# Optimization experiments

Hardware: AMD Instinct MI355X
Metric: run time of the kernel (lower is better)

Reference implementation:

```python
import jax, jax.numpy as jnp
import numpy as np

TS = (32, 32, 32)          # tensor_size per dim
NC = 32 * 32 * 32          # total grid cells
HEADS = 4


def setup_inputs() -> dict:
    key = jax.random.key(0)
    k1, k2, k3 = jax.random.split(key, 3)
    B, H, V, N = 4, HEADS, 8, 16384
    local_coordinate = jax.random.uniform(k1, (B, H, V, N), dtype=jnp.float32)
    flattened_index = jax.random.randint(k2, (B, H, V, N), 0, NC, dtype=jnp.int64)
    features = jax.random.normal(k3, (B, 128, N), dtype=jnp.float32)
    return {"local_coordinate": local_coordinate,
            "flattened_index": flattened_index,
            "features": features}


def reference(local_coordinate, flattened_index, features):
    # local_coordinate: [B, H, V, N], flattened_index: [B, H, V, N] int64
    # features: [B, H*fd, N]
    B, H, V, N = local_coordinate.shape
    fd = features.shape[1] // H
    feats = features.reshape(B, H, fd, N)
    # outer-product splat: [B, H, fd, V, N]
    pre_splat = feats[:, :, :, None, :] * local_coordinate[:, :, None, :, :]
    src = pre_splat.reshape(B, H, fd, V * N)
    idx = flattened_index.reshape(B, H, V * N)

    def scat(s, i):
        # s: [fd, V*N], i: [V*N]; out initialized to zeros like torch scatter_max with zero out
        return jnp.zeros((fd, NC), dtype=s.dtype).at[:, i].max(s)

    z = jax.vmap(jax.vmap(scat))(src, idx)  # [B, H, fd, NC]
    return z.reshape(B, H * fd, *TS)
```

## Files before the change

kernel.cpp:

```cpp
#include <hip/hip_runtime.h>
#include <hip/hip_bf16.h>

constexpr int B  = 4;
constexpr int H  = 4;
constexpr int V  = 8;
constexpr int N  = 16384;
constexpr int FD = 32;
constexpr int NC = 32768;
constexpr int BH = B * H;
constexpr int VN = V * N;
constexpr int NPAIR = BH * VN;

constexpr int CB   = 1024;
constexpr int CAPB = 208;
constexpr int TP   = 8192;
constexpr int SB   = NPAIR / TP;
constexpr int TB   = BH * (N / 128);

constexpr size_t OFF_BCNT   = 0;
constexpr size_t OFF_SLOTS  = OFF_BCNT  + (size_t)BH * CB;
constexpr size_t OFF_FEATST = OFF_SLOTS + (size_t)BH * CB * CAPB;

__device__ __forceinline__ unsigned short f2bf(float v) {
    unsigned int u = __float_as_uint(v);
    return (unsigned short)((u + 0x7FFFu + ((u >> 16) & 1u)) >> 16);
}

__global__ __launch_bounds__(1024)
void k_prep(const int* __restrict__ idx, const float* __restrict__ lc,
            const float* __restrict__ feats, int* __restrict__ bcnt,
            unsigned int* __restrict__ slots, unsigned short* __restrict__ featsT) {
    __shared__ __align__(16) unsigned char smem[61440];
    const int tid = threadIdx.x;

    if (blockIdx.x < SB) {
        unsigned int*   skey   = (unsigned int*)smem;
        unsigned short* scb    = (unsigned short*)(smem + 32768);
        int*            s      = (int*)(smem + 49152);
        int*            cursor = (int*)(smem + 53248);
        int*            rbase  = (int*)(smem + 57344);

        const size_t t0 = (size_t)blockIdx.x * TP;
        const int bh = (int)(t0 >> 17);

        s[tid] = 0;
        __syncthreads();

        const int4* idx4 = (const int4*)(idx + t0);
        int4 c4a[2];
#pragma unroll
        for (int r = 0; r < 2; ++r) {
            int4 c4 = idx4[tid + r * 1024];
            c4a[r] = c4;
            atomicAdd(&s[c4.x >> 5], 1);
            atomicAdd(&s[c4.y >> 5], 1);
            atomicAdd(&s[c4.z >> 5], 1);
            atomicAdd(&s[c4.w >> 5], 1);
        }
        __syncthreads();
        const int myc = s[tid];

        for (int off = 1; off < 1024; off <<= 1) {
            int v = (tid >= off) ? s[tid - off] : 0;
            __syncthreads();
            s[tid] += v;
            __syncthreads();
        }
        const int scanstart = s[tid] - myc;
        __syncthreads();
        s[tid]      = scanstart;
        cursor[tid] = scanstart;
        rbase[tid]  = (myc > 0) ? atomicAdd(&bcnt[bh * CB + tid], myc) : 0;
        __syncthreads();

        const float4* lc4 = (const float4*)(lc + t0);
        const unsigned int nb = (unsigned int)(t0 & (N - 1));
#pragma unroll
        for (int r = 0; r < 2; ++r) {
            int i = tid + r * 1024;
            int4   c4 = c4a[r];
            float4 l4 = lc4[i];
            unsigned int n0 = nb + (unsigned int)(i * 4);
            int cx[4] = {c4.x, c4.y, c4.z, c4.w};
            float lx[4] = {l4.x, l4.y, l4.z, l4.w};
#pragma unroll
            for (int e = 0; e < 4; ++e) {
                unsigned int q = (unsigned int)(lx[e] * 8192.0f);
                unsigned int key = ((unsigned int)(cx[e] & 31) << 27)
                                 | (q << 14) | (n0 + e);
                int cb = cx[e] >> 5;
                int pos = atomicAdd(&cursor[cb], 1);
                skey[pos] = key;
                scb[pos]  = (unsigned short)cb;
            }
        }
        __syncthreads();

#pragma unroll
        for (int r = 0; r < 8; ++r) {
            int j  = tid + r * 1024;
            int cb = scb[j];
            int gpos = rbase[cb] + (j - s[cb]);
            if (gpos < CAPB)
                slots[((size_t)bh * CB + cb) * CAPB + gpos] = skey[j];
        }
    } else {
        float (*tile)[32][33] = (float (*)[32][33])smem;
        int bi  = blockIdx.x - SB;
        int bh  = bi >> 7;
        int n0  = (bi & 127) * 128;
        int sub = tid >> 8;
        int tx  = tid & 31;
        int ty  = (tid >> 5) & 7;
        int nb  = n0 + sub * 32;
#pragma unroll
        for (int fr = 0; fr < 4; ++fr) {
            int f = ty + fr * 8;
            tile[sub][f][tx] = feats[((size_t)bh * FD + f) * N + nb + tx];
        }
        __syncthreads();
#pragma unroll
        for (int nr = 0; nr < 4; ++nr) {
            int n = ty + nr * 8;
            featsT[((size_t)bh * N + nb + n) * FD + tx] = f2bf(tile[sub][tx][n]);
        }
    }
}

__global__ __launch_bounds__(256)
void k_compute(const int* __restrict__ bcnt, const unsigned int* __restrict__ slots,
               const unsigned short* __restrict__ featsT, float* __restrict__ out) {
    __shared__ unsigned int acc[32][33];
    __shared__ unsigned int kbuf[CAPB];
    const int tid = threadIdx.x;
    const int bh  = blockIdx.x >> 10;
    const int cb  = blockIdx.x & (CB - 1);

    int cnt = bcnt[bh * CB + cb];
    if (cnt > CAPB) cnt = CAPB;
    const unsigned int* row = slots + ((size_t)bh * CB + cb) * CAPB;
    if (tid < cnt) kbuf[tid] = row[tid];
    for (int i = tid; i < 32 * 33; i += 256) ((unsigned int*)acc)[i] = 0u;
    __syncthreads();

    const int g = tid >> 5;
    const int f = tid & 31;
    const unsigned short* fT = featsT + (size_t)bh * N * FD;
    const int last = cnt - 1;

    for (int r0 = 8 * g; r0 < cnt; r0 += 64) {
        unsigned int k[8];
        float fv[8];
#pragma unroll
        for (int j = 0; j < 8; ++j)
            k[j] = kbuf[min(r0 + j, last)];
#pragma unroll
        for (int j = 0; j < 8; ++j) {
            int off = (int)((k[j] & 16383u) << 5) | f;
            fv[j] = __uint_as_float((unsigned int)fT[off] << 16);
        }
#pragma unroll
        for (int j = 0; j < 8; ++j) {
            float coord = ((float)((k[j] >> 14) & 8191u) + 0.5f) * (1.0f / 8192.0f);
            float val = fmaxf(coord * fv[j], 0.0f);
            atomicMax(&acc[k[j] >> 27][f], __float_as_uint(val));
        }
    }
    __syncthreads();

    int cell = tid & 31;
    int c0   = cb * 32;
#pragma unroll
    for (int i = 0; i < 4; ++i) {
        int ff = (tid >> 5) + i * 8;
        __builtin_nontemporal_store(__uint_as_float(acc[cell][ff]),
            &out[((size_t)(bh * FD + ff)) * NC + c0 + cell]);
    }
}

extern "C" void kernel_launch(void* const* d_in, const int* in_sizes, int n_in,
                              void* d_out, int out_size, void* d_ws, size_t ws_size,
                              hipStream_t stream) {
    const float* lc    = (const float*)d_in[0];
    const int*   idx   = (const int*)  d_in[1];
    const float* feats = (const float*)d_in[2];
    float* out = (float*)d_out;

    int*            bcnt   = (int*)d_ws + OFF_BCNT;
    unsigned int*   slots  = (unsigned int*)d_ws + OFF_SLOTS;
    unsigned short* featsT = (unsigned short*)((unsigned int*)d_ws + OFF_FEATST);

    hipMemsetAsync(bcnt, 0, (size_t)BH * CB * sizeof(int), stream);

    k_prep<<<SB + TB, 1024, 0, stream>>>(idx, lc, feats, bcnt, slots, featsT);
    k_compute<<<BH * CB, 256, 0, stream>>>(bcnt, slots, featsT, out);
}
```

Before: 138.0 us.

## Use wave-shuffle scan, sort keys by cell, merge runs before atomics, vectorize stores

The 1024-entry block scan in the prep kernel, which used shared memory and many barriers, becomes a two-level wavefront shuffle scan. In the compute kernel, each bucket's keys are counting-sorted by cell within the block. Consecutive keys for the same cell are then max-reduced in registers, so fewer shared atomicMax calls are issued, and non-positive values skip the atomic entirely. Output stores become 4-wide vector nontemporal stores. The cost is an extra histogram/scan/scatter phase with more barriers per compute block.

```diff
diff --git a/kernel.cpp b/kernel.cpp
--- a/kernel.cpp
+++ b/kernel.cpp
@@ -21,6 +21,8 @@
 constexpr size_t OFF_SLOTS  = OFF_BCNT  + (size_t)BH * CB;
 constexpr size_t OFF_FEATST = OFF_SLOTS + (size_t)BH * CB * CAPB;
 
+typedef float f32x4 __attribute__((ext_vector_type(4)));
+
 __device__ __forceinline__ unsigned short f2bf(float v) {
     unsigned int u = __float_as_uint(v);
     return (unsigned short)((u + 0x7FFFu + ((u >> 16) & 1u)) >> 16);
@@ -60,14 +62,30 @@
         __syncthreads();
         const int myc = s[tid];
 
-        for (int off = 1; off < 1024; off <<= 1) {
-            int v = (tid >= off) ? s[tid - off] : 0;
-            __syncthreads();
-            s[tid] += v;
-            __syncthreads();
-        }
-        const int scanstart = s[tid] - myc;
-        __syncthreads();
+        const int lane = tid & 63;
+        const int wid  = tid >> 6;
+        int inc = myc;
+#pragma unroll
+        for (int off = 1; off < 64; off <<= 1) {
+            int t = __shfl_up(inc, off, 64);
+            if (lane >= off) inc += t;
+        }
+        if (lane == 63) cursor[wid] = inc;
+        __syncthreads();
+        if (tid < 16) {
+            int wv = cursor[tid];
+            int winc = wv;
+#pragma unroll
+            for (int off = 1; off < 16; off <<= 1) {
+                int t = __shfl_up(winc, off, 64);
+                if (tid >= off) winc += t;
+            }
+            cursor[16 + tid] = winc - wv;
+        }
+        __syncthreads();
+        const int scanstart = cursor[16 + wid] + inc - myc;
+        __syncthreads();
+
         s[tid]      = scanstart;
         cursor[tid] = scanstart;
         rbase[tid]  = (myc > 0) ? atomicAdd(&bcnt[bh * CB + tid], myc) : 0;
@@ -132,6 +150,9 @@
                const unsigned short* __restrict__ featsT, float* __restrict__ out) {
     __shared__ unsigned int acc[32][33];
     __shared__ unsigned int kbuf[CAPB];
+    __shared__ unsigned int skb[CAPB];
+    __shared__ int chist[32];
+    __shared__ int ccur[32];
     const int tid = threadIdx.x;
     const int bh  = blockIdx.x >> 10;
     const int cb  = blockIdx.x & (CB - 1);
@@ -139,8 +160,29 @@
     int cnt = bcnt[bh * CB + cb];
     if (cnt > CAPB) cnt = CAPB;
     const unsigned int* row = slots + ((size_t)bh * CB + cb) * CAPB;
+    if (tid < 32) chist[tid] = 0;
     if (tid < cnt) kbuf[tid] = row[tid];
     for (int i = tid; i < 32 * 33; i += 256) ((unsigned int*)acc)[i] = 0u;
+    __syncthreads();
+
+    if (tid < cnt) atomicAdd(&chist[kbuf[tid] >> 27], 1);
+    __syncthreads();
+    if (tid < 64) {
+        int c = (tid < 32) ? chist[tid] : 0;
+        int inc = c;
+#pragma unroll
+        for (int off = 1; off < 32; off <<= 1) {
+            int t = __shfl_up(inc, off, 64);
+            if (tid >= off) inc += t;
+        }
+        if (tid < 32) ccur[tid] = inc - c;
+    }
+    __syncthreads();
+    if (tid < cnt) {
+        unsigned int key = kbuf[tid];
+        int p = atomicAdd(&ccur[key >> 27], 1);
+        skb[p] = key;
+    }
     __syncthreads();
 
     const int g = tid >> 5;
@@ -153,29 +195,43 @@
         float fv[8];
 #pragma unroll
         for (int j = 0; j < 8; ++j)
-            k[j] = kbuf[min(r0 + j, last)];
+            k[j] = skb[min(r0 + j, last)];
 #pragma unroll
         for (int j = 0; j < 8; ++j) {
             int off = (int)((k[j] & 16383u) << 5) | f;
             fv[j] = __uint_as_float((unsigned int)fT[off] << 16);
         }
+        float val[8];
 #pragma unroll
         for (int j = 0; j < 8; ++j) {
             float coord = ((float)((k[j] >> 14) & 8191u) + 0.5f) * (1.0f / 8192.0f);
-            float val = fmaxf(coord * fv[j], 0.0f);
-            atomicMax(&acc[k[j] >> 27][f], __float_as_uint(val));
-        }
-    }
-    __syncthreads();
-
-    int cell = tid & 31;
-    int c0   = cb * 32;
-#pragma unroll
-    for (int i = 0; i < 4; ++i) {
-        int ff = (tid >> 5) + i * 8;
-        __builtin_nontemporal_store(__uint_as_float(acc[cell][ff]),
-            &out[((size_t)(bh * FD + ff)) * NC + c0 + cell]);
-    }
+            val[j] = coord * fv[j];
+        }
+        float run = val[0];
+#pragma unroll
+        for (int j = 1; j < 8; ++j) {
+            if ((k[j] >> 27) == (k[j - 1] >> 27)) {
+                run = fmaxf(run, val[j]);
+            } else {
+                if (run > 0.0f)
+                    atomicMax(&acc[k[j - 1] >> 27][f], __float_as_uint(run));
+                run = val[j];
+            }
+        }
+        if (run > 0.0f)
+            atomicMax(&acc[k[7] >> 27][f], __float_as_uint(run));
+    }
+    __syncthreads();
+
+    const int ff = tid >> 3;
+    const int c4 = (tid & 7) * 4;
+    f32x4 o;
+    o.x = __uint_as_float(acc[c4 + 0][ff]);
+    o.y = __uint_as_float(acc[c4 + 1][ff]);
+    o.z = __uint_as_float(acc[c4 + 2][ff]);
+    o.w = __uint_as_float(acc[c4 + 3][ff]);
+    __builtin_nontemporal_store(o,
+        reinterpret_cast<f32x4*>(&out[((size_t)(bh * FD + ff)) * NC + cb * 32 + c4]));
 }
 
 extern "C" void kernel_launch(void* const* d_in, const int* in_sizes, int n_in,
```

Result: slower. 146.9 us (+6.4%).

## Use wave-shuffle scan, paired bf16 gathers, and vectorized output stores

Applied to the files above, without the earlier changes.

The block-wide prefix scan in the prep kernel now uses wavefront shuffles plus a small cross-wave scan in place of a log-step shared-memory scan with barriers. In the compute kernel each lane gathers two bf16 features as one 32-bit load and handles 16 lanes per entry, which halves the number of gather instructions. The output is written with 16-byte nontemporal vector stores in place of scalar stores. Each thread now issues two LDS atomics per entry, and the per-thread unroll drops from 8 to 4 entries, which lowers memory-level parallelism per thread.

```diff
diff --git a/kernel.cpp b/kernel.cpp
--- a/kernel.cpp
+++ b/kernel.cpp
@@ -21,6 +21,8 @@
 constexpr size_t OFF_SLOTS  = OFF_BCNT  + (size_t)BH * CB;
 constexpr size_t OFF_FEATST = OFF_SLOTS + (size_t)BH * CB * CAPB;
 
+typedef float f32x4 __attribute__((ext_vector_type(4)));
+
 __device__ __forceinline__ unsigned short f2bf(float v) {
     unsigned int u = __float_as_uint(v);
     return (unsigned short)((u + 0x7FFFu + ((u >> 16) & 1u)) >> 16);
@@ -60,14 +62,30 @@
         __syncthreads();
         const int myc = s[tid];
 
-        for (int off = 1; off < 1024; off <<= 1) {
-            int v = (tid >= off) ? s[tid - off] : 0;
-            __syncthreads();
-            s[tid] += v;
-            __syncthreads();
-        }
-        const int scanstart = s[tid] - myc;
-        __syncthreads();
+        const int lane = tid & 63;
+        const int wid  = tid >> 6;
+        int inc = myc;
+#pragma unroll
+        for (int off = 1; off < 64; off <<= 1) {
+            int t = __shfl_up(inc, off, 64);
+            if (lane >= off) inc += t;
+        }
+        if (lane == 63) cursor[wid] = inc;
+        __syncthreads();
+        if (tid < 16) {
+            int wv = cursor[tid];
+            int winc = wv;
+#pragma unroll
+            for (int off = 1; off < 16; off <<= 1) {
+                int t = __shfl_up(winc, off, 64);
+                if (tid >= off) winc += t;
+            }
+            cursor[16 + tid] = winc - wv;
+        }
+        __syncthreads();
+        const int scanstart = cursor[16 + wid] + inc - myc;
+        __syncthreads();
+
         s[tid]      = scanstart;
         cursor[tid] = scanstart;
         rbase[tid]  = (myc > 0) ? atomicAdd(&bcnt[bh * CB + tid], myc) : 0;
@@ -143,39 +161,43 @@
     for (int i = tid; i < 32 * 33; i += 256) ((unsigned int*)acc)[i] = 0u;
     __syncthreads();
 
-    const int g = tid >> 5;
-    const int f = tid & 31;
-    const unsigned short* fT = featsT + (size_t)bh * N * FD;
+    const int gi = tid >> 4;
+    const int fl = tid & 15;
+    const unsigned int* fT32 = (const unsigned int*)(featsT + (size_t)bh * N * FD);
     const int last = cnt - 1;
 
-    for (int r0 = 8 * g; r0 < cnt; r0 += 64) {
-        unsigned int k[8];
-        float fv[8];
-#pragma unroll
-        for (int j = 0; j < 8; ++j)
+    for (int r0 = 4 * gi; r0 < cnt; r0 += 64) {
+        unsigned int k[4];
+        unsigned int w[4];
+#pragma unroll
+        for (int j = 0; j < 4; ++j)
             k[j] = kbuf[min(r0 + j, last)];
 #pragma unroll
-        for (int j = 0; j < 8; ++j) {
-            int off = (int)((k[j] & 16383u) << 5) | f;
-            fv[j] = __uint_as_float((unsigned int)fT[off] << 16);
-        }
-#pragma unroll
-        for (int j = 0; j < 8; ++j) {
+        for (int j = 0; j < 4; ++j)
+            w[j] = fT32[(int)((k[j] & 16383u) << 4) | fl];
+#pragma unroll
+        for (int j = 0; j < 4; ++j) {
             float coord = ((float)((k[j] >> 14) & 8191u) + 0.5f) * (1.0f / 8192.0f);
-            float val = fmaxf(coord * fv[j], 0.0f);
-            atomicMax(&acc[k[j] >> 27][f], __float_as_uint(val));
+            float f0 = __uint_as_float(w[j] << 16);
+            float f1 = __uint_as_float(w[j] & 0xFFFF0000u);
+            float v0 = fmaxf(coord * f0, 0.0f);
+            float v1 = fmaxf(coord * f1, 0.0f);
+            unsigned int* a = &acc[k[j] >> 27][fl * 2];
+            atomicMax(&a[0], __float_as_uint(v0));
+            atomicMax(&a[1], __float_as_uint(v1));
         }
     }
     __syncthreads();
 
-    int cell = tid & 31;
-    int c0   = cb * 32;
-#pragma unroll
-    for (int i = 0; i < 4; ++i) {
-        int ff = (tid >> 5) + i * 8;
-        __builtin_nontemporal_store(__uint_as_float(acc[cell][ff]),
-            &out[((size_t)(bh * FD + ff)) * NC + c0 + cell]);
-    }
+    const int ff = tid >> 3;
+    const int c4 = (tid & 7) * 4;
+    f32x4 o;
+    o.x = __uint_as_float(acc[c4 + 0][ff]);
+    o.y = __uint_as_float(acc[c4 + 1][ff]);
+    o.z = __uint_as_float(acc[c4 + 2][ff]);
+    o.w = __uint_as_float(acc[c4 + 3][ff]);
+    __builtin_nontemporal_store(o,
+        reinterpret_cast<f32x4*>(&out[((size_t)(bh * FD + ff)) * NC + cb * 32 + c4]));
 }
 
 extern "C" void kernel_launch(void* const* d_in, const int* in_sizes, int n_in,
```

Measured after the change: 135.5 us. No clear change (-1.8%).
